# Optimization experiments

Hardware: AMD Instinct MI355X
Metric: run time of the kernel (lower is better)

Reference implementation:

```python
import jax, jax.numpy as jnp
import numpy as np

B, L, D = 4, 512, 2880          # packed sequences, tokens per seq, hidden
N, K, H = 64, 8, 64             # query heads, kv heads, head dim
G = N // K                      # GQA group size
WINDOW = 128                    # sliding window (gpt-oss window layer)
SM_SCALE = 1.0 / H ** 0.5
THETA = 150000.0
INIT_CTX = 4096.0
SCALING = 32.0
NTK_ALPHA = 1.0
NTK_BETA = 32.0
NEG = -1e30


def _rope_tables(positions):
    # GPT-OSS YaRN NTK-by-parts rotary tables.
    d_half = H // 2
    freq = THETA ** (jnp.arange(0, H, 2, dtype=jnp.float32) / H)
    concentration = 0.1 * np.log(SCALING) + 1.0
    low = d_half * np.log(INIT_CTX / (NTK_BETA * 2 * np.pi)) / np.log(THETA)
    high = d_half * np.log(INIT_CTX / (NTK_ALPHA * 2 * np.pi)) / np.log(THETA)
    interp = 1.0 / (SCALING * freq)
    extrap = 1.0 / freq
    ramp = jnp.clip((jnp.arange(d_half, dtype=jnp.float32) - low) / (high - low), 0.0, 1.0)
    blend = 1.0 - ramp
    inv_freq = interp * (1.0 - blend) + extrap * blend
    ang = positions.astype(jnp.float32)[:, None] * inv_freq[None, :]  # [T, H/2]
    return jnp.cos(ang) * concentration, jnp.sin(ang) * concentration


def _apply_rope(x, cos, sin):
    # x: [T, heads, H]; half-split rotation as in gpt-oss.
    x1, x2 = x[..., : H // 2], x[..., H // 2:]
    c, s = cos[:, None, :], sin[:, None, :]
    return jnp.concatenate([x1 * c - x2 * s, x2 * c + x1 * s], axis=-1)


def setup_inputs() -> dict:
    key = jax.random.key(0)
    ks = jax.random.split(key, 10)
    T = B * L
    return {
        "x": jax.random.normal(ks[0], (T, D), jnp.float32),
        "wq": jax.random.normal(ks[1], (D, N, H), jnp.float32) * 0.02,
        "bq": jax.random.normal(ks[2], (N, H), jnp.float32) * 0.02,
        "wk": jax.random.normal(ks[3], (D, K, H), jnp.float32) * 0.02,
        "bk": jax.random.normal(ks[4], (K, H), jnp.float32) * 0.02,
        "wv": jax.random.normal(ks[5], (D, K, H), jnp.float32) * 0.02,
        "bv": jax.random.normal(ks[6], (K, H), jnp.float32) * 0.02,
        "wo": jax.random.normal(ks[7], (N, H, D), jnp.float32) * 0.02,
        "bo": jax.random.normal(ks[8], (D,), jnp.float32) * 0.02,
        "sinks": jax.random.normal(ks[9], (N,), jnp.float32),
        "positions": jnp.tile(jnp.arange(L, dtype=jnp.int32), B),  # per-seq positions
    }


def reference(x, wq, bq, wk, bk, wv, bv, wo, bo, sinks, positions):
    # fused QKV projections
    q = jnp.einsum('td,dnh->tnh', x, wq) + bq            # [T,N,H]
    k = jnp.einsum('td,dkh->tkh', x, wk) + bk            # [T,K,H]
    v = jnp.einsum('td,dkh->tkh', x, wv) + bv            # [T,K,H]
    cos, sin = _rope_tables(positions)
    q = _apply_rope(q, cos, sin)
    k = _apply_rope(k, cos, sin)
    # unpack ragged tokens into [B, L, ...] (equal-length packed sequences)
    qb = q.reshape(B, L, K, G, H)
    kb = k.reshape(B, L, K, H)
    vb = v.reshape(B, L, K, H)
    s = jnp.einsum('blkgh,bmkh->bkglm', qb, kb) * SM_SCALE  # [B,K,G,L,L]
    pos = jnp.arange(L)
    delta = pos[:, None] - pos[None, :]
    allowed = (delta >= 0) & (delta < WINDOW)               # causal + sliding window
    s = jnp.where(allowed, s, NEG)
    # attention sinks: extra per-head logit joining the softmax denominator only
    sink = sinks.reshape(K, G)[None, :, :, None]            # [1,K,G,1]
    m = jnp.maximum(jnp.max(s, axis=-1), sink)              # [B,K,G,L]
    p = jnp.exp(s - m[..., None])
    denom = jnp.exp(sink - m) + jnp.sum(p, axis=-1)         # [B,K,G,L]
    o = jnp.einsum('bkglm,bmkh->blkgh', p, vb)
    o = o / jnp.transpose(denom, (0, 3, 1, 2))[..., None]   # [B,L,K,G,H]
    attn = o.reshape(B * L, N, H)
    return jnp.einsum('tnh,nhd->td', attn, wo) + bo         # [T,D]
```

## Files before the change

kernel.cpp:

```cpp
#include <hip/hip_runtime.h>
#include <hip/hip_bf16.h>

#define TB 4
#define TL 512
#define TD 2880
#define TN 64
#define TKH 8
#define TH 64
#define TG 8
#define TWIN 128
#define TT (TB*TL)

typedef unsigned short u16;
typedef __attribute__((ext_vector_type(8))) short bf16x8;
typedef __attribute__((ext_vector_type(4))) float f32x4;

__device__ __forceinline__ u16 f2b(float f) {
  unsigned u = __float_as_uint(f);
  u += 0x7fffu + ((u >> 16) & 1u);
  return (u16)(u >> 16);
}
__device__ __forceinline__ float b2f(u16 u) {
  return __uint_as_float(((unsigned)u) << 16);
}

__device__ __forceinline__ void load_lds16(const u16* g, u16* l) {
  __builtin_amdgcn_global_load_lds(
      (const __attribute__((address_space(1))) unsigned int*)g,
      (__attribute__((address_space(3))) unsigned int*)l, 16, 0, 0);
}

template<int BN, int ROPE>
__global__ __launch_bounds__(256, 6) void gemm_db(
    const u16* __restrict__ A, const u16* __restrict__ Bt,
    const float* __restrict__ bias, void* __restrict__ Cv,
    const int* __restrict__ positions,
    int Kd, int Nc, int ldc, int out_bf16, int nx)
{
  constexpr int NF = BN / 32;
  __shared__ u16 As[2][128*32];
  __shared__ u16 Bs[2][BN*32];

  const int tid  = threadIdx.x;
  const int lane = tid & 63;
  const int wave = tid >> 6;

  int id = blockIdx.x;
  const int cpx = gridDim.x >> 3;
  id = (id & 7)*cpx + (id >> 3);
  const int rgsz = nx << 3;
  const int rg   = id / rgsz;
  const int rem  = id - rg*rgsz;
  const int bm = (rg*8 + (rem & 7)) * 128;
  const int bn = (rem >> 3) * BN;

  const int wr = (wave >> 1) * 64;
  const int wc = ROPE ? (wave & 1) * 16 : (wave & 1) * (BN/2);
  constexpr int NSTR = ROPE ? 32 : 16;

  f32x4 acc[4][NF];
#pragma unroll
  for (int i = 0; i < 4; ++i)
#pragma unroll
    for (int j = 0; j < NF; ++j) acc[i][j] = (f32x4){0.f,0.f,0.f,0.f};

  const int rr   = tid >> 2;
  const int sseg = (tid & 3) ^ ((rr >> 1) & 3);
  const u16* aS = A  + (size_t)(bm + rr)*Kd + sseg*8;
  const u16* bS = Bt + (size_t)(bn + rr)*Kd + sseg*8;

#define STG(dc, kt) do {                                         \
    const int _k0 = (kt) << 5;                                   \
    load_lds16(aS + _k0,                    &As[dc][wave*512]);  \
    load_lds16(aS + (size_t)64*Kd + _k0,    &As[dc][2048 + wave*512]); \
    load_lds16(bS + _k0,                    &Bs[dc][wave*512]);  \
  } while (0)

  const int fr = lane & 15, kq = lane >> 4;
  const int sx = (fr >> 1) & 3;

  const int NT = Kd >> 5;
  STG(0, 0);

  for (int t = 0; t < NT; ++t) {
    const int c = t & 1;
    if (t + 1 < NT) {
      STG(c ^ 1, t + 1);
      asm volatile("s_waitcnt vmcnt(3)" ::: "memory");
    } else {
      asm volatile("s_waitcnt vmcnt(0)" ::: "memory");
    }
    __builtin_amdgcn_s_barrier();
    __builtin_amdgcn_sched_barrier(0);

    bf16x8 af[4], bv[NF];
#pragma unroll
    for (int mi = 0; mi < 4; ++mi) {
      const int row = wr + mi*16 + fr;
      af[mi] = *(const bf16x8*)((const char*)&As[c][row*32] + ((kq ^ sx) << 4));
    }
#pragma unroll
    for (int ni = 0; ni < NF; ++ni) {
      const int row = wc + ni*NSTR + fr;
      bv[ni] = *(const bf16x8*)((const char*)&Bs[c][row*32] + ((kq ^ sx) << 4));
    }
    __builtin_amdgcn_s_setprio(1);
#pragma unroll
    for (int mi = 0; mi < 4; ++mi)
#pragma unroll
      for (int ni = 0; ni < NF; ++ni)
        acc[mi][ni] = __builtin_amdgcn_mfma_f32_16x16x32_bf16(
            af[mi], bv[ni], acc[mi][ni], 0, 0, 0);
    __builtin_amdgcn_s_setprio(0);

    __builtin_amdgcn_s_barrier();
    __builtin_amdgcn_sched_barrier(0);
  }
#undef STG

  const int rbase = bm + wr + (lane >> 4)*4;

  if (ROPE) {
    const int i = wc + (lane & 15);
    const int col1 = bn + i, col2 = col1 + 32;
    const int htype = (bn < 4096) ? 0 : (bn < 4608 ? 1 : 2);
    const float b1 = bias[col1], b2 = bias[col2];

    float invf = 0.f, mul = 0.f;
    if (htype < 2) {
      const float lnth = 11.918390573078392f;
      const float low  = 8.092779f;
      const float high = 17.398025f;
      const float conc = 1.3465735903f;
      const float fi = (float)i * 0.03125f;
      const float itp = __expf(-fi * lnth);
      float ramp = ((float)i - low) * (1.0f/(high - low));
      ramp = fminf(fmaxf(ramp, 0.0f), 1.0f);
      invf = itp*(1.0f/32.0f)*ramp + itp*(1.0f - ramp);
      mul = (htype == 0) ? (conc * 0.125f) : conc;
    }

    u16* Cb = (u16*)Cv;
#pragma unroll
    for (int mi = 0; mi < 4; ++mi) {
#pragma unroll
      for (int j = 0; j < 4; ++j) {
        const int row = rbase + mi*16 + j;
        float x1 = acc[mi][0][j] + b1;
        float x2 = acc[mi][1][j] + b2;
        if (htype < 2) {
          const float ang = (float)positions[row] * invf;
          const float cc = cosf(ang) * mul;
          const float ss = sinf(ang) * mul;
          const float y1 = x1*cc - x2*ss;
          const float y2 = x2*cc + x1*ss;
          x1 = y1; x2 = y2;
        }
        Cb[(size_t)row*ldc + col1] = f2b(x1);
        Cb[(size_t)row*ldc + col2] = f2b(x2);
      }
    }
  } else {
    const int cbase = bn + wc + (lane & 15);
#pragma unroll
    for (int mi = 0; mi < 4; ++mi) {
#pragma unroll
      for (int ni = 0; ni < NF; ++ni) {
        const int col = cbase + ni*NSTR;
        const float bvl = (col < Nc) ? bias[col] : 0.f;
#pragma unroll
        for (int j = 0; j < 4; ++j) {
          const int row = rbase + mi*16 + j;
          const float val = acc[mi][ni][j] + bvl;
          if (out_bf16) {
            ((u16*)Cv)[(size_t)row*ldc + col] = f2b(val);
          } else if (col < Nc) {
            ((float*)Cv)[(size_t)row*ldc + col] = val;
          }
        }
      }
    }
  }
}

__device__ __forceinline__ void tconv_into(
    float (*tile)[33], const float* __restrict__ in, u16* __restrict__ out,
    int R, int C, int bx, int by, int tid)
{
  const int c0 = bx*32, r0 = by*32;
  const int tx = tid & 31, ty = tid >> 5;
#pragma unroll
  for (int i = 0; i < 4; ++i)
    tile[ty + i*8][tx] = in[(size_t)(r0 + ty + i*8)*C + c0 + tx];
  __syncthreads();
#pragma unroll
  for (int i = 0; i < 4; ++i) {
    const int oc = ty + i*8;
    out[(size_t)(c0 + oc)*R + r0 + tx] = f2b(tile[tx][oc]);
  }
}

__global__ __launch_bounds__(256) void prep_kernel(
    const float* __restrict__ x,  const float* __restrict__ wq,
    const float* __restrict__ wk, const float* __restrict__ wv,
    const float* __restrict__ wo, const float* __restrict__ bq,
    const float* __restrict__ bk, const float* __restrict__ bv,
    u16* __restrict__ xb, u16* __restrict__ wqkvt, u16* __restrict__ wot,
    float* __restrict__ bqkv)
{
  __shared__ float tile[32][33];
  const int b = blockIdx.x;
  const int tid = threadIdx.x;

  if (b < 5760) {
    const int i = b*256 + tid;
    float4 f = ((const float4*)x)[i];
    ushort4 o;
    o.x = f2b(f.x); o.y = f2b(f.y); o.z = f2b(f.z); o.w = f2b(f.w);
    ((ushort4*)xb)[i] = o;
  } else if (b < 17280) {
    const int local = b - 5760;
    tconv_into(tile, wq, wqkvt, TD, 4096, local % 128, local / 128, tid);
  } else if (b < 18720) {
    const int local = b - 17280;
    tconv_into(tile, wk, wqkvt + (size_t)4096*TD, TD, 512,
               local % 16, local / 16, tid);
  } else if (b < 20160) {
    const int local = b - 18720;
    tconv_into(tile, wv, wqkvt + (size_t)4608*TD, TD, 512,
               local % 16, local / 16, tid);
  } else if (b < 31680) {
    const int local = b - 20160;
    tconv_into(tile, wo, wot, 4096, TD, local % 90, local / 90, tid);
  } else if (b < 31936) {
    const int i = (b - 31680)*256 + tid;
    ((ushort4*)(wot + (size_t)2880*4096))[i] = (ushort4){0,0,0,0};
  } else {
    const int i = (b - 31936)*256 + tid;
    if (i < 5120)
      bqkv[i] = (i < 4096) ? bq[i] : (i < 4608 ? bk[i-4096] : bv[i-4608]);
  }
}

__global__ __launch_bounds__(512) void attn3_kernel(
    const u16* __restrict__ qkv, u16* __restrict__ obuf,
    const float* __restrict__ sinks)
{
  __shared__ u16 Kl[192*64];
  __shared__ u16 Vt[64*192];
  __shared__ u16 Pl[8][2048];

  const int lt = blockIdx.x, kh = blockIdx.y, b = blockIdx.z;
  const int l0 = lt*64;
  const int mstart = (l0 > 127) ? (l0 - 127) : 0;
  const int mcnt = l0 + 64 - mstart;
  const int NC = (mcnt + 31) >> 5;
  const int base = l0 - mstart;

  const int tid = threadIdx.x;
  const int lane = tid & 63;
  const int g = tid >> 6;
  const int lL = lane & 15;
  const int q = lane >> 4;

  {
    const u16* kv0 = qkv + ((size_t)(b*TL + mstart)*5120 + 4096 + kh*64);
    for (int s = tid; s < 1536; s += 512) {
      const int m = s >> 3, hs = s & 7;
      uint4 kx = make_uint4(0,0,0,0), vx = make_uint4(0,0,0,0);
      if (m < mcnt) {
        const u16* gp = kv0 + (size_t)m*5120 + hs*8;
        kx = *(const uint4*)gp;
        vx = *(const uint4*)(gp + 512);
      }
      *(uint4*)((char*)&Kl[m*64] + ((hs*16) ^ ((m&7)<<4))) = kx;
      const unsigned vw[4] = {vx.x, vx.y, vx.z, vx.w};
#pragma unroll
      for (int i = 0; i < 8; ++i) {
        const int h = hs*8 + i;
        const u16 val = (u16)(vw[i>>1] >> ((i&1)*16));
        *(u16*)((char*)&Vt[h*192] + ((m*2) ^ (((h>>3)&7)<<4))) = val;
      }
    }
  }

  bf16x8 qb[4][2];
  {
    const u16* qbase = qkv + ((size_t)(b*TL + l0)*5120 + (kh*8 + g)*64);
#pragma unroll
    for (int l4 = 0; l4 < 4; ++l4)
#pragma unroll
      for (int kk = 0; kk < 2; ++kk)
        qb[l4][kk] = *(const bf16x8*)(qbase + (size_t)(l4*16 + lL)*5120 + kk*32 + q*8);
  }
  const float sink = sinks[kh*8 + g];
  __syncthreads();

  float Mrun[4] = {-1e30f,-1e30f,-1e30f,-1e30f};
  float Dden[4] = {0.f,0.f,0.f,0.f};
  f32x4 oacc[4][4];
#pragma unroll
  for (int i = 0; i < 4; ++i)
#pragma unroll
    for (int j = 0; j < 4; ++j) oacc[i][j] = (f32x4){0.f,0.f,0.f,0.f};

  u16* Pw = &Pl[g][0];

  for (int c = 0; c < NC; ++c) {
    bf16x8 ka[2][2];
#pragma unroll
    for (int m2 = 0; m2 < 2; ++m2) {
      const int row = c*32 + m2*16 + lL;
#pragma unroll
      for (int kk = 0; kk < 2; ++kk)
        ka[m2][kk] = *(const bf16x8*)((char*)&Kl[row*64] +
                       ((kk*64 + q*16) ^ ((row&7)<<4)));
    }
    bf16x8 vb[4];
#pragma unroll
    for (int hf = 0; hf < 4; ++hf) {
      const int h = hf*16 + lL;
      vb[hf] = *(const bf16x8*)((char*)&Vt[h*192] +
                 ((c*64 + q*16) ^ (((h>>3)&7)<<4)));
    }

#pragma unroll
    for (int l4 = 0; l4 < 4; ++l4) {
      const int lo = base + l4*16;
      if (c*32 > lo + 15 || c*32 + 31 < lo - 127) continue;

      const f32x4 z = (f32x4){0.f,0.f,0.f,0.f};
      f32x4 s0 = __builtin_amdgcn_mfma_f32_16x16x32_bf16(ka[0][0], qb[l4][0], z, 0,0,0);
      s0 = __builtin_amdgcn_mfma_f32_16x16x32_bf16(ka[0][1], qb[l4][1], s0, 0,0,0);
      f32x4 s1 = __builtin_amdgcn_mfma_f32_16x16x32_bf16(ka[1][0], qb[l4][0], z, 0,0,0);
      s1 = __builtin_amdgcn_mfma_f32_16x16x32_bf16(ka[1][1], qb[l4][1], s1, 0,0,0);

      float sv[2][4];
      bool  al[2][4];
      float cmax = -1e30f;
#pragma unroll
      for (int m2 = 0; m2 < 2; ++m2)
#pragma unroll
        for (int j = 0; j < 4; ++j) {
          const int delta = (lo + lL) - (c*32 + m2*16 + q*4 + j);
          const bool a = (delta >= 0) && (delta < TWIN);
          const float s = (m2 ? s1[j] : s0[j]);
          sv[m2][j] = s;
          al[m2][j] = a;
          if (a) cmax = fmaxf(cmax, s);
        }
      cmax = fmaxf(cmax, __shfl_xor(cmax, 16));
      cmax = fmaxf(cmax, __shfl_xor(cmax, 32));
      const float Mn = fmaxf(Mrun[l4], cmax);
      const float r = __expf(Mrun[l4] - Mn);
      Mrun[l4] = Mn;

      float ls = 0.f;
      u16 pb[2][4];
#pragma unroll
      for (int m2 = 0; m2 < 2; ++m2)
#pragma unroll
        for (int j = 0; j < 4; ++j) {
          const float p = al[m2][j] ? __expf(sv[m2][j] - Mn) : 0.f;
          ls += p;
          pb[m2][j] = f2b(p);
        }
      ls += __shfl_xor(ls, 16);
      ls += __shfl_xor(ls, 32);
      Dden[l4] = Dden[l4]*r + ls;

      const int l = l4*16 + lL;
#pragma unroll
      for (int m2 = 0; m2 < 2; ++m2) {
        uint2 w;
        w.x = (unsigned)pb[m2][0] | ((unsigned)pb[m2][1] << 16);
        w.y = (unsigned)pb[m2][2] | ((unsigned)pb[m2][3] << 16);
        *(uint2*)((char*)Pw + l*64 + ((m2*32 + q*8) ^ ((l&3)<<4))) = w;
      }

      float rb[4];
#pragma unroll
      for (int j = 0; j < 4; ++j) rb[j] = __shfl(r, q*4 + j);
#pragma unroll
      for (int hf = 0; hf < 4; ++hf)
#pragma unroll
        for (int j = 0; j < 4; ++j) oacc[l4][hf][j] *= rb[j];

      bf16x8 pa = *(const bf16x8*)((char*)Pw + l*64 + ((q*16) ^ ((l&3)<<4)));
#pragma unroll
      for (int hf = 0; hf < 4; ++hf)
        oacc[l4][hf] = __builtin_amdgcn_mfma_f32_16x16x32_bf16(
            pa, vb[hf], oacc[l4][hf], 0, 0, 0);
    }
  }

#pragma unroll
  for (int l4 = 0; l4 < 4; ++l4) {
    const float di = 1.0f / (Dden[l4] + __expf(sink - Mrun[l4]));
    float db[4];
#pragma unroll
    for (int j = 0; j < 4; ++j) db[j] = __shfl(di, q*4 + j);
#pragma unroll
    for (int hf = 0; hf < 4; ++hf)
#pragma unroll
      for (int j = 0; j < 4; ++j) {
        const int row = l0 + l4*16 + q*4 + j;
        obuf[(size_t)(b*TL + row)*4096 + (kh*8 + g)*64 + hf*16 + lL] =
            f2b(oacc[l4][hf][j] * db[j]);
      }
  }
}

extern "C" void kernel_launch(void* const* d_in, const int* in_sizes, int n_in,
                              void* d_out, int out_size, void* d_ws, size_t ws_size,
                              hipStream_t stream)
{
  const float* x     = (const float*)d_in[0];
  const float* wq    = (const float*)d_in[1];
  const float* bq    = (const float*)d_in[2];
  const float* wk    = (const float*)d_in[3];
  const float* bk    = (const float*)d_in[4];
  const float* wv    = (const float*)d_in[5];
  const float* bv    = (const float*)d_in[6];
  const float* wo    = (const float*)d_in[7];
  const float* bo    = (const float*)d_in[8];
  const float* sinks = (const float*)d_in[9];
  const int* positions = (const int*)d_in[10];
  float* out = (float*)d_out;

  u16* xb    = (u16*)d_ws;
  u16* wqkvt = xb + (size_t)TT*TD;
  u16* wot   = wqkvt + (size_t)5120*TD;
  u16* qkv   = wot + (size_t)2944*4096;
  u16* obuf  = qkv + (size_t)TT*5120;
  float* bqkv = (float*)(obuf + (size_t)TT*4096);

  prep_kernel<<<31956, 256, 0, stream>>>(
      x, wq, wk, wv, wo, bq, bk, bv, xb, wqkvt, wot, bqkv);

  gemm_db<64, 1><<<1280, 256, 0, stream>>>(
      xb, wqkvt, bqkv, qkv, positions, TD, 5120, 5120, 1, 80);

  attn3_kernel<<<dim3(8, TKH, TB), 512, 0, stream>>>(qkv, obuf, sinks);

  gemm_db<64, 0><<<720, 256, 0, stream>>>(
      obuf, wot, bo, out, nullptr, 4096, 2880, 2880, 0, 45);
}
```

Before: 233.0 us.

## Replace double-buffered BK=32 GEMM loop with single-buffer BK=64 loop

Both GEMMs drop the double-buffered 32-wide K pipeline, with its explicit vmcnt waits and priority hints, for a single LDS buffer that stages 64 K elements per iteration. Each iteration loads the tile, synchronizes, runs two MFMA sub-steps, and synchronizes again. The LDS row swizzle widens to an 8-way XOR to fit the wider rows, and the launch-bounds occupancy hint drops from 6 to 4. The goal is fewer barriers and loop iterations per tile, but global loads no longer overlap with MFMA work inside a block, so latency hiding now depends on other resident blocks.

```diff
diff --git a/kernel.cpp b/kernel.cpp
--- a/kernel.cpp
+++ b/kernel.cpp
@@ -31,15 +31,15 @@
 }
 
 template<int BN, int ROPE>
-__global__ __launch_bounds__(256, 6) void gemm_db(
+__global__ __launch_bounds__(256, 4) void gemm_sn(
     const u16* __restrict__ A, const u16* __restrict__ Bt,
     const float* __restrict__ bias, void* __restrict__ Cv,
     const int* __restrict__ positions,
     int Kd, int Nc, int ldc, int out_bf16, int nx)
 {
   constexpr int NF = BN / 32;
-  __shared__ u16 As[2][128*32];
-  __shared__ u16 Bs[2][BN*32];
+  __shared__ u16 As[128*64];
+  __shared__ u16 Bs[BN*64];
 
   const int tid  = threadIdx.x;
   const int lane = tid & 63;
@@ -64,59 +64,48 @@
 #pragma unroll
     for (int j = 0; j < NF; ++j) acc[i][j] = (f32x4){0.f,0.f,0.f,0.f};
 
-  const int rr   = tid >> 2;
-  const int sseg = (tid & 3) ^ ((rr >> 1) & 3);
+  const int rr   = tid >> 3;
+  const int sseg = (tid & 7) ^ (rr & 7);
   const u16* aS = A  + (size_t)(bm + rr)*Kd + sseg*8;
   const u16* bS = Bt + (size_t)(bn + rr)*Kd + sseg*8;
 
-#define STG(dc, kt) do {                                         \
-    const int _k0 = (kt) << 5;                                   \
-    load_lds16(aS + _k0,                    &As[dc][wave*512]);  \
-    load_lds16(aS + (size_t)64*Kd + _k0,    &As[dc][2048 + wave*512]); \
-    load_lds16(bS + _k0,                    &Bs[dc][wave*512]);  \
-  } while (0)
-
   const int fr = lane & 15, kq = lane >> 4;
-  const int sx = (fr >> 1) & 3;
-
-  const int NT = Kd >> 5;
-  STG(0, 0);
-
+  const int swz = lane & 7;
+
+  const int NT = Kd >> 6;
   for (int t = 0; t < NT; ++t) {
-    const int c = t & 1;
-    if (t + 1 < NT) {
-      STG(c ^ 1, t + 1);
-      asm volatile("s_waitcnt vmcnt(3)" ::: "memory");
-    } else {
-      asm volatile("s_waitcnt vmcnt(0)" ::: "memory");
-    }
-    __builtin_amdgcn_s_barrier();
-    __builtin_amdgcn_sched_barrier(0);
-
-    bf16x8 af[4], bv[NF];
-#pragma unroll
-    for (int mi = 0; mi < 4; ++mi) {
-      const int row = wr + mi*16 + fr;
-      af[mi] = *(const bf16x8*)((const char*)&As[c][row*32] + ((kq ^ sx) << 4));
-    }
-#pragma unroll
-    for (int ni = 0; ni < NF; ++ni) {
-      const int row = wc + ni*NSTR + fr;
-      bv[ni] = *(const bf16x8*)((const char*)&Bs[c][row*32] + ((kq ^ sx) << 4));
-    }
-    __builtin_amdgcn_s_setprio(1);
-#pragma unroll
-    for (int mi = 0; mi < 4; ++mi)
-#pragma unroll
-      for (int ni = 0; ni < NF; ++ni)
-        acc[mi][ni] = __builtin_amdgcn_mfma_f32_16x16x32_bf16(
-            af[mi], bv[ni], acc[mi][ni], 0, 0, 0);
-    __builtin_amdgcn_s_setprio(0);
-
-    __builtin_amdgcn_s_barrier();
-    __builtin_amdgcn_sched_barrier(0);
-  }
-#undef STG
+    const int k0 = t << 6;
+#pragma unroll
+    for (int i = 0; i < 4; ++i)
+      load_lds16(aS + (size_t)i*32*Kd + k0, &As[i*2048 + wave*512]);
+#pragma unroll
+    for (int i = 0; i < BN/32; ++i)
+      load_lds16(bS + (size_t)i*32*Kd + k0, &Bs[i*2048 + wave*512]);
+    __syncthreads();
+
+#pragma unroll
+    for (int s = 0; s < 2; ++s) {
+      const int ch = ((s*4 + kq) ^ swz) * 16;
+      bf16x8 af[4], bv[NF];
+#pragma unroll
+      for (int mi = 0; mi < 4; ++mi) {
+        const int row = wr + mi*16 + fr;
+        af[mi] = *(const bf16x8*)((const char*)&As[row*64] + ch);
+      }
+#pragma unroll
+      for (int ni = 0; ni < NF; ++ni) {
+        const int row = wc + ni*NSTR + fr;
+        bv[ni] = *(const bf16x8*)((const char*)&Bs[row*64] + ch);
+      }
+#pragma unroll
+      for (int mi = 0; mi < 4; ++mi)
+#pragma unroll
+        for (int ni = 0; ni < NF; ++ni)
+          acc[mi][ni] = __builtin_amdgcn_mfma_f32_16x16x32_bf16(
+              af[mi], bv[ni], acc[mi][ni], 0, 0, 0);
+    }
+    __syncthreads();
+  }
 
   const int rbase = bm + wr + (lane >> 4)*4;
 
@@ -438,11 +427,11 @@
   prep_kernel<<<31956, 256, 0, stream>>>(
       x, wq, wk, wv, wo, bq, bk, bv, xb, wqkvt, wot, bqkv);
 
-  gemm_db<64, 1><<<1280, 256, 0, stream>>>(
+  gemm_sn<64, 1><<<1280, 256, 0, stream>>>(
       xb, wqkvt, bqkv, qkv, positions, TD, 5120, 5120, 1, 80);
 
   attn3_kernel<<<dim3(8, TKH, TB), 512, 0, stream>>>(qkv, obuf, sinks);
 
-  gemm_db<64, 0><<<720, 256, 0, stream>>>(
+  gemm_sn<64, 0><<<720, 256, 0, stream>>>(
       obuf, wot, bo, out, nullptr, 4096, 2880, 2880, 0, 45);
 }
```

New measurement: 199.5 us. 1.17x faster.
